# Performance work log

Hardware: AMD Instinct MI355X
Metric: run time of the kernel (lower is better)

Reference implementation:

```python
import jax, jax.numpy as jnp
import numpy as np

N_NODES = 50000
N_EDGES = 600000
D_IN = 128
H = D_IN // 2  # 64
N_GRAPHS = 500
DIM_TARGET = 1


def setup_inputs() -> dict:
    key = jax.random.key(0)
    ks = jax.random.split(key, 16)
    x = jax.random.normal(ks[0], (N_NODES, D_IN), dtype=jnp.float32)
    edge_index = jax.random.randint(ks[1], (2, N_EDGES), 0, N_NODES, dtype=jnp.int64)
    batch = jnp.sort(jax.random.randint(ks[2], (N_NODES,), 0, N_GRAPHS, dtype=jnp.int64))
    # SAGEConv params: lin_l (neighbor aggregate, with bias), lin_r (root, no bias)
    s = 1.0 / np.sqrt(D_IN)
    Wl = jax.random.uniform(ks[3], (D_IN, H), jnp.float32, -s, s)
    bl = jnp.zeros((H,), jnp.float32)
    Wr = jax.random.uniform(ks[4], (D_IN, H), jnp.float32, -s, s)
    # MLP: 64->32->16->8->1
    dims = [H, H // 2, H // 4, H // 8, DIM_TARGET]
    params = {}
    for i in range(4):
        si = 1.0 / np.sqrt(dims[i])
        params[f"W{i}"] = jax.random.uniform(ks[5 + 2 * i], (dims[i], dims[i + 1]), jnp.float32, -si, si)
        params[f"b{i}"] = jax.random.uniform(ks[6 + 2 * i], (dims[i + 1],), jnp.float32, -si, si)
    return dict(x=x, edge_index=edge_index, batch=batch, Wl=Wl, bl=bl, Wr=Wr, **params)


def reference(x, edge_index, batch, Wl, bl, Wr, W0, b0, W1, b1, W2, b2, W3, b3):
    n_nodes = x.shape[0]
    src, dst = edge_index[0], edge_index[1]
    # SAGEConv mean aggregation: mean of source-node features at each target node
    agg = jax.ops.segment_sum(x[src], dst, num_segments=n_nodes)          # [N, D]
    cnt = jax.ops.segment_sum(jnp.ones((src.shape[0],), x.dtype), dst, num_segments=n_nodes)
    mean_nbr = agg / jnp.maximum(cnt, 1.0)[:, None]
    x1 = mean_nbr @ Wl + bl + x @ Wr                                      # [N, H]
    # global_mean_pool by graph id
    gsum = jax.ops.segment_sum(x1, batch, num_segments=N_GRAPHS)          # [G, H]
    gcnt = jax.ops.segment_sum(jnp.ones((n_nodes,), x.dtype), batch, num_segments=N_GRAPHS)
    h = gsum / jnp.maximum(gcnt, 1.0)[:, None]
    # MLP (dropout is identity in eval mode)
    h = jax.nn.relu(h @ W0 + b0)
    h = jax.nn.relu(h @ W1 + b1)
    h = jax.nn.relu(h @ W2 + b2)
    return h @ W3 + b3
```

## Files before the change

kernel.cpp:

```cpp
#include <hip/hip_runtime.h>
#include <hip/hip_bf16.h>

#define N_NODES  50000
#define N_EDGES  600000
#define D_IN     128
#define H        64
#define N_GRAPHS 500
#define MAXDEG   48

#define PROJ_BLOCKS 782
#define M_TILES     3125
#define SCAT_CHUNKS 512
#define SCAT_BLOCKS (SCAT_CHUNKS * 8)
#define EPC         1172
#define NPS         (N_NODES / 8)
#define GST_BLOCKS  2
#define PREP_GRID   (PROJ_BLOCKS + SCAT_BLOCKS + GST_BLOCKS)

#define SPLIT    16
#define GBLK     (N_GRAPHS * SPLIT)

#define OF_DEG   0
#define MEMSET_B 200704
#define OF_PNP   200704
#define OF_GST   4296704
#define OF_COL   4298752
#define OF_YB    9098752
#define OF_ZB    15498752

typedef __attribute__((ext_vector_type(8))) short short8;
typedef __attribute__((ext_vector_type(4))) float float4v;

__device__ __forceinline__ float bflo(unsigned int u) { return __uint_as_float(u << 16); }
__device__ __forceinline__ float bfhi(unsigned int u) { return __uint_as_float(u & 0xffff0000u); }
__device__ __forceinline__ unsigned short f2bf(float f) {
    return __bfloat16_as_ushort(__float2bfloat16(f));
}

__global__ __launch_bounds__(256) void prep_kernel(
        const float* __restrict__ x, const float* __restrict__ Wl,
        const float* __restrict__ Wr,
        unsigned short* __restrict__ yb, unsigned short* __restrict__ zb,
        const int* __restrict__ src, const int* __restrict__ dst,
        int* __restrict__ deg, unsigned short* __restrict__ col,
        const int* __restrict__ batch, int* __restrict__ gstart) {
    int bid = blockIdx.x, t = threadIdx.x;
    int wave = t >> 6, lane = t & 63;

    if (bid < PROJ_BLOCKS) {
        int mt = bid * 4 + wave;
        if (mt < M_TILES) {
            int c = lane & 15, q = lane >> 4;
            float4v accY[4] = {};
            float4v accZ[4] = {};
            const float* xrow = x + ((size_t)mt * 16 + c) * D_IN + q * 8;
            #pragma unroll
            for (int s4 = 0; s4 < 4; ++s4) {
                const float4* ap = (const float4*)(xrow + s4 * 32);
                float4 a0 = ap[0], a1 = ap[1];
                short8 Af;
                Af[0] = (short)f2bf(a0.x); Af[1] = (short)f2bf(a0.y);
                Af[2] = (short)f2bf(a0.z); Af[3] = (short)f2bf(a0.w);
                Af[4] = (short)f2bf(a1.x); Af[5] = (short)f2bf(a1.y);
                Af[6] = (short)f2bf(a1.z); Af[7] = (short)f2bf(a1.w);
                int kb = s4 * 32 + q * 8;
                #pragma unroll
                for (int t4 = 0; t4 < 4; ++t4) {
                    const float* wl = Wl + (size_t)kb * H + t4 * 16 + c;
                    const float* wr = Wr + (size_t)kb * H + t4 * 16 + c;
                    short8 BL, BR;
                    #pragma unroll
                    for (int jj = 0; jj < 8; ++jj) {
                        BL[jj] = (short)f2bf(wl[jj * H]);
                        BR[jj] = (short)f2bf(wr[jj * H]);
                    }
                    accY[t4] = __builtin_amdgcn_mfma_f32_16x16x32_bf16(Af, BL, accY[t4], 0, 0, 0);
                    accZ[t4] = __builtin_amdgcn_mfma_f32_16x16x32_bf16(Af, BR, accZ[t4], 0, 0, 0);
                }
            }
            #pragma unroll
            for (int t4 = 0; t4 < 4; ++t4)
                #pragma unroll
                for (int r = 0; r < 4; ++r) {
                    int node = mt * 16 + q * 4 + r;
                    yb[(size_t)node * H + t4 * 16 + c] = f2bf(accY[t4][r]);
                    zb[(size_t)node * H + t4 * 16 + c] = f2bf(accZ[t4][r]);
                }
        }
    } else if (bid < PROJ_BLOCKS + SCAT_BLOCKS) {
        int shard = bid & 7;
        int chunk = (bid - PROJ_BLOCKS) >> 3;
        int lo = shard * NPS, hi = lo + NPS;
        int e0 = chunk * EPC;
        int e1 = e0 + EPC; if (e1 > N_EDGES) e1 = N_EDGES;
        for (int e = e0 + t; e < e1; e += 256) {
            int d = dst[e];
            if (d >= lo && d < hi) {
                int pos = atomicAdd(&deg[d], 1);
                if (pos < MAXDEG)
                    col[(size_t)d * MAXDEG + pos] = (unsigned short)src[e];
            }
        }
    } else {
        int g = (bid - PROJ_BLOCKS - SCAT_BLOCKS) * 256 + t;
        if (g <= N_GRAPHS) {
            int lo = 0, hi = N_NODES;
            while (lo < hi) {
                int m = (lo + hi) >> 1;
                if (batch[m] < g) lo = m + 1; else hi = m;
            }
            gstart[g] = lo;
        }
    }
}

__global__ __launch_bounds__(256) void gather_kernel(
        const unsigned short* __restrict__ yb, const unsigned short* __restrict__ zb,
        const unsigned short* __restrict__ col,
        const int* __restrict__ deg, const int* __restrict__ gstart,
        float* __restrict__ PnP) {
    __shared__ float red[8 * H];
    int bid  = blockIdx.x;
    int wave = threadIdx.x >> 6;
    int lane = threadIdx.x & 63;
    int half = lane >> 5, fp = lane & 31;
    int g = bid >> 4, s = bid & 15;
    int n0 = gstart[g], n1 = gstart[g + 1];
    const unsigned short* yl = yb + 2 * fp;

    float2 pn = make_float2(0.f, 0.f);
    float2 pz = make_float2(0.f, 0.f);
    for (int n = n0 + s * 4 + wave; n < n1; n += 4 * SPLIT) {
        unsigned int uz = *(const unsigned int*)(zb + (size_t)n * H + 2 * fp);
        pz.x += bflo(uz); pz.y += bfhi(uz);

        int d = deg[n];
        int dl = (d < MAXDEG) ? d : MAXDEG;
        int cidx = (lane < dl) ? (int)col[(size_t)n * MAXDEG + lane] : 0;

        float tx = 0.f, ty = 0.f;
        int j = 0;
        for (; j + 8 <= dl; j += 8) {
            int s0 = __shfl(cidx, j + half),     s1 = __shfl(cidx, j + 2 + half);
            int s2 = __shfl(cidx, j + 4 + half), s3 = __shfl(cidx, j + 6 + half);
            unsigned int u0 = *(const unsigned int*)(yl + (size_t)s0 * H);
            unsigned int u1 = *(const unsigned int*)(yl + (size_t)s1 * H);
            unsigned int u2 = *(const unsigned int*)(yl + (size_t)s2 * H);
            unsigned int u3 = *(const unsigned int*)(yl + (size_t)s3 * H);
            tx += bflo(u0) + bflo(u1) + bflo(u2) + bflo(u3);
            ty += bfhi(u0) + bfhi(u1) + bfhi(u2) + bfhi(u3);
        }
        for (; j + 2 <= dl; j += 2) {
            int s0 = __shfl(cidx, j + half);
            unsigned int u = *(const unsigned int*)(yl + (size_t)s0 * H);
            tx += bflo(u); ty += bfhi(u);
        }
        if (j < dl) {
            int s0 = __shfl(cidx, j);
            if (half == 0) {
                unsigned int u = *(const unsigned int*)(yl + (size_t)s0 * H);
                tx += bflo(u); ty += bfhi(u);
            }
        }
        if (d > 0) {
            float w = __builtin_amdgcn_rcpf((float)d);
            pn.x = fmaf(tx, w, pn.x);
            pn.y = fmaf(ty, w, pn.y);
        }
    }
    pn.x += __shfl_xor(pn.x, 32);
    pn.y += __shfl_xor(pn.y, 32);
    pz.x += __shfl_xor(pz.x, 32);
    pz.y += __shfl_xor(pz.y, 32);
    if (half == 0) {
        red[wave * H + 2 * fp]             = pn.x;
        red[wave * H + 2 * fp + 1]         = pn.y;
        red[4 * H + wave * H + 2 * fp]     = pz.x * 0.5f;
        red[4 * H + wave * H + 2 * fp + 1] = pz.y * 0.5f;
    }
    __syncthreads();
    if (threadIdx.x < H) {
        int i = threadIdx.x;
        float v = red[i] + red[H + i] + red[2 * H + i] + red[3 * H + i];
        PnP[(size_t)bid * 2 * H + i] = v;
    } else if (threadIdx.x < 2 * H) {
        int i = threadIdx.x - H;
        float v = red[4 * H + i] + red[5 * H + i] + red[6 * H + i] + red[7 * H + i];
        PnP[(size_t)bid * 2 * H + H + i] = v;
    }
}

__global__ void final_kernel(
        const float* __restrict__ PnP, const int* __restrict__ gstart,
        const float* __restrict__ bl,
        const float* __restrict__ W0, const float* __restrict__ b0,
        const float* __restrict__ W1, const float* __restrict__ b1,
        const float* __restrict__ W2, const float* __restrict__ b2,
        const float* __restrict__ W3, const float* __restrict__ b3,
        float* __restrict__ out) {
    int g = blockIdx.x;
    int t = threadIdx.x;
    __shared__ float hs[H], a0[32], a1[16], a2[8];
    float sy = 0.f, sz = 0.f;
    {
        const float* base = PnP + ((size_t)g << 4) * 2 * H;
        #pragma unroll
        for (int s = 0; s < SPLIT; ++s) {
            sy += base[s * 2 * H + t];
            sz += base[s * 2 * H + H + t];
        }
    }
    int ng = gstart[g + 1] - gstart[g];
    hs[t] = (ng > 0) ? ((sy + sz) / (float)ng + bl[t]) : 0.f;
    __syncthreads();
    if (t < 32) { float a = b0[t]; for (int d = 0; d < H;  ++d) a += hs[d] * W0[d * 32 + t]; a0[t] = fmaxf(a, 0.f); }
    __syncthreads();
    if (t < 16) { float a = b1[t]; for (int d = 0; d < 32; ++d) a += a0[d] * W1[d * 16 + t]; a1[t] = fmaxf(a, 0.f); }
    __syncthreads();
    if (t < 8)  { float a = b2[t]; for (int d = 0; d < 16; ++d) a += a1[d] * W2[d * 8 + t];  a2[t] = fmaxf(a, 0.f); }
    __syncthreads();
    if (t == 0) { float a = b3[0]; for (int d = 0; d < 8;  ++d) a += a2[d] * W3[d]; out[g] = a; }
}

extern "C" void kernel_launch(void* const* d_in, const int* in_sizes, int n_in,
                              void* d_out, int out_size, void* d_ws, size_t ws_size,
                              hipStream_t stream) {
    const float* x     = (const float*)d_in[0];
    const int*   ei    = (const int*)  d_in[1];
    const int*   batch = (const int*)  d_in[2];
    const float* Wl    = (const float*)d_in[3];
    const float* bl    = (const float*)d_in[4];
    const float* Wr    = (const float*)d_in[5];
    const float* W0    = (const float*)d_in[6];
    const float* b0    = (const float*)d_in[7];
    const float* W1    = (const float*)d_in[8];
    const float* b1    = (const float*)d_in[9];
    const float* W2    = (const float*)d_in[10];
    const float* b2    = (const float*)d_in[11];
    const float* W3    = (const float*)d_in[12];
    const float* b3    = (const float*)d_in[13];
    float* out = (float*)d_out;

    char* ws = (char*)d_ws;
    int*            deg    = (int*)(ws + OF_DEG);
    float*          PnP    = (float*)(ws + OF_PNP);
    int*            gstart = (int*)(ws + OF_GST);
    unsigned short* col    = (unsigned short*)(ws + OF_COL);
    unsigned short* yb     = (unsigned short*)(ws + OF_YB);
    unsigned short* zb     = (unsigned short*)(ws + OF_ZB);

    hipMemsetAsync(ws, 0, MEMSET_B, stream);

    prep_kernel<<<PREP_GRID, 256, 0, stream>>>(
        x, Wl, Wr, yb, zb, ei, ei + N_EDGES, deg, col, batch, gstart);
    gather_kernel<<<GBLK, 256, 0, stream>>>(yb, zb, col, deg, gstart, PnP);
    final_kernel<<<N_GRAPHS, 64, 0, stream>>>(PnP, gstart, bl,
                                              W0, b0, W1, b1, W2, b2, W3, b3, out);
}
```

Before: 163.0 us.

## Stage bf16 weights and x tile in LDS, coalesce projection output stores

The projection blocks now convert Wl and Wr to bf16 once per block into padded, transposed LDS tiles and stage each wave's 16-row x tile in LDS. MFMA operands are then read with vector LDS loads instead of the strided per-element global weight loads done before. Results are routed through LDS so each lane writes 16-byte contiguous chunks of yb and zb. The cost is that every block reloads and converts the full weight matrices and adds a __syncthreads. The larger shared memory footprint also applies to the scatter blocks, which may reduce their occupancy.

```diff
diff --git a/kernel.cpp b/kernel.cpp
--- a/kernel.cpp
+++ b/kernel.cpp
@@ -8,8 +8,8 @@
 #define N_GRAPHS 500
 #define MAXDEG   48
 
+#define M_TILES     3125
 #define PROJ_BLOCKS 782
-#define M_TILES     3125
 #define SCAT_CHUNKS 512
 #define SCAT_BLOCKS (SCAT_CHUNKS * 8)
 #define EPC         1172
@@ -19,6 +19,13 @@
 
 #define SPLIT    16
 #define GBLK     (N_GRAPHS * SPLIT)
+
+#define BSTRIDE 136
+#define BOFF    (64 * BSTRIDE)
+#define AOFF    (2 * BOFF)
+#define AWAVE   (16 * BSTRIDE)
+#define LDS_SH  (AOFF + 4 * AWAVE)
+#define OSTRIDE 72
 
 #define OF_DEG   0
 #define MEMSET_B 200704
@@ -29,6 +36,7 @@
 #define OF_ZB    15498752
 
 typedef __attribute__((ext_vector_type(8))) short short8;
+typedef __attribute__((ext_vector_type(8))) unsigned short ushort8v;
 typedef __attribute__((ext_vector_type(4))) float float4v;
 
 __device__ __forceinline__ float bflo(unsigned int u) { return __uint_as_float(u << 16); }
@@ -44,48 +52,76 @@
         const int* __restrict__ src, const int* __restrict__ dst,
         int* __restrict__ deg, unsigned short* __restrict__ col,
         const int* __restrict__ batch, int* __restrict__ gstart) {
+    __shared__ unsigned short lds[LDS_SH];
     int bid = blockIdx.x, t = threadIdx.x;
     int wave = t >> 6, lane = t & 63;
 
     if (bid < PROJ_BLOCKS) {
-        int mt = bid * 4 + wave;
-        if (mt < M_TILES) {
+        #pragma unroll 4
+        for (int i = t; i < H * D_IN; i += 256) {
+            int k = i >> 6, h = i & 63;
+            lds[h * BSTRIDE + k]        = f2bf(Wl[i]);
+            lds[BOFF + h * BSTRIDE + k] = f2bf(Wr[i]);
+        }
+        int task = bid * 4 + wave;
+        bool active = (task < M_TILES);
+        unsigned short* At = lds + AOFF + wave * AWAVE;
+        if (active) {
+            int r = lane >> 2, cg = lane & 3;
+            const float* xr = x + ((size_t)task * 16 + r) * D_IN;
+            #pragma unroll
+            for (int i = 0; i < 4; ++i) {
+                int c0 = (cg + 4 * i) * 8;
+                float4 f0 = *(const float4*)(xr + c0);
+                float4 f1 = *(const float4*)(xr + c0 + 4);
+                ushort8v v;
+                v[0] = f2bf(f0.x); v[1] = f2bf(f0.y); v[2] = f2bf(f0.z); v[3] = f2bf(f0.w);
+                v[4] = f2bf(f1.x); v[5] = f2bf(f1.y); v[6] = f2bf(f1.z); v[7] = f2bf(f1.w);
+                *(ushort8v*)(At + r * BSTRIDE + c0) = v;
+            }
+        }
+        __syncthreads();
+        if (active) {
             int c = lane & 15, q = lane >> 4;
             float4v accY[4] = {};
             float4v accZ[4] = {};
-            const float* xrow = x + ((size_t)mt * 16 + c) * D_IN + q * 8;
             #pragma unroll
             for (int s4 = 0; s4 < 4; ++s4) {
-                const float4* ap = (const float4*)(xrow + s4 * 32);
-                float4 a0 = ap[0], a1 = ap[1];
-                short8 Af;
-                Af[0] = (short)f2bf(a0.x); Af[1] = (short)f2bf(a0.y);
-                Af[2] = (short)f2bf(a0.z); Af[3] = (short)f2bf(a0.w);
-                Af[4] = (short)f2bf(a1.x); Af[5] = (short)f2bf(a1.y);
-                Af[6] = (short)f2bf(a1.z); Af[7] = (short)f2bf(a1.w);
-                int kb = s4 * 32 + q * 8;
+                short8 Af = *(short8*)(At + c * BSTRIDE + s4 * 32 + q * 8);
                 #pragma unroll
                 for (int t4 = 0; t4 < 4; ++t4) {
-                    const float* wl = Wl + (size_t)kb * H + t4 * 16 + c;
-                    const float* wr = Wr + (size_t)kb * H + t4 * 16 + c;
-                    short8 BL, BR;
+                    int hrow = (t4 * 16 + c) * BSTRIDE + s4 * 32 + q * 8;
+                    short8 BLf = *(short8*)(lds + hrow);
+                    short8 BRf = *(short8*)(lds + BOFF + hrow);
+                    accY[t4] = __builtin_amdgcn_mfma_f32_16x16x32_bf16(Af, BLf, accY[t4], 0, 0, 0);
+                    accZ[t4] = __builtin_amdgcn_mfma_f32_16x16x32_bf16(Af, BRf, accZ[t4], 0, 0, 0);
+                }
+            }
+            int rr = lane >> 2, cg2 = lane & 3;
+            {
+                #pragma unroll
+                for (int t4 = 0; t4 < 4; ++t4)
                     #pragma unroll
-                    for (int jj = 0; jj < 8; ++jj) {
-                        BL[jj] = (short)f2bf(wl[jj * H]);
-                        BR[jj] = (short)f2bf(wr[jj * H]);
-                    }
-                    accY[t4] = __builtin_amdgcn_mfma_f32_16x16x32_bf16(Af, BL, accY[t4], 0, 0, 0);
-                    accZ[t4] = __builtin_amdgcn_mfma_f32_16x16x32_bf16(Af, BR, accZ[t4], 0, 0, 0);
-                }
-            }
-            #pragma unroll
-            for (int t4 = 0; t4 < 4; ++t4)
+                    for (int r2 = 0; r2 < 4; ++r2)
+                        At[(q * 4 + r2) * OSTRIDE + t4 * 16 + c] = f2bf(accY[t4][r2]);
+                ushort8v o0 = *(ushort8v*)(At + rr * OSTRIDE + cg2 * 16);
+                ushort8v o1 = *(ushort8v*)(At + rr * OSTRIDE + cg2 * 16 + 8);
+                unsigned short* op = yb + ((size_t)task * 16 + rr) * H + cg2 * 16;
+                *(ushort8v*)op       = o0;
+                *(ushort8v*)(op + 8) = o1;
+            }
+            {
                 #pragma unroll
-                for (int r = 0; r < 4; ++r) {
-                    int node = mt * 16 + q * 4 + r;
-                    yb[(size_t)node * H + t4 * 16 + c] = f2bf(accY[t4][r]);
-                    zb[(size_t)node * H + t4 * 16 + c] = f2bf(accZ[t4][r]);
-                }
+                for (int t4 = 0; t4 < 4; ++t4)
+                    #pragma unroll
+                    for (int r2 = 0; r2 < 4; ++r2)
+                        At[(q * 4 + r2) * OSTRIDE + t4 * 16 + c] = f2bf(accZ[t4][r2]);
+                ushort8v o0 = *(ushort8v*)(At + rr * OSTRIDE + cg2 * 16);
+                ushort8v o1 = *(ushort8v*)(At + rr * OSTRIDE + cg2 * 16 + 8);
+                unsigned short* op = zb + ((size_t)task * 16 + rr) * H + cg2 * 16;
+                *(ushort8v*)op       = o0;
+                *(ushort8v*)(op + 8) = o1;
+            }
         }
     } else if (bid < PROJ_BLOCKS + SCAT_BLOCKS) {
         int shard = bid & 7;
```

After: 160.2 us. No clear change (-1.7%).
